# Kernel optimization log

Measured on AMD Instinct MI355X. Metric: run time of the kernel, lower is better.

The kernel has to match this reference:

```python
import jax, jax.numpy as jnp
import numpy as np

# pywt db4 reconstruction low-pass (rec_lo) coefficients.
_H = np.array([
    0.23037781330885523, 0.7148465705525415, 0.6308807679295904,
    -0.02798376941698385, -0.18703481171888114, 0.030841381835986965,
    0.032883011666982945, -0.010597401784997278], dtype=np.float64)
# pywt dec_lo = _H[::-1]; conv (flipped) correlation kernel = dec_lo[::-1] = _H.
_FLO = _H
# dec_hi[k] = (-1)^(7-k) * _H[k]; correlation kernel = dec_hi[::-1] -> (-1)^k * _H[7-k].
_FHI = np.array([(-1.0) ** k * _H[7 - k] for k in range(8)])
_FILT = jnp.asarray(np.stack([_FLO, _FHI])[:, None, :], dtype=jnp.float32)  # [2,1,8]
_PAD = 7  # filter_len - 1
_LEVEL = 4


def _dwt_step(sig):
    """One pywt dwt level, mode='symmetric'. sig: [N, L] -> (cA, cD), each [N, (L+7)//2]."""
    # symmetric (half-sample) extension by filter_len-1 each side, drop first sample
    # so that stride-2 VALID correlation reproduces pywt's output phase/length.
    xp = jnp.pad(sig, ((0, 0), (_PAD, _PAD)), mode='symmetric')[:, 1:]
    out = jax.lax.conv_general_dilated(
        xp[:, None, :], _FILT, window_strides=(2,), padding='VALID',
        dimension_numbers=('NCH', 'OIH', 'NCH'))  # [N, 2, (L+7)//2]
    return out[:, 0, :], out[:, 1, :]


def setup_inputs() -> dict:
    key = jax.random.key(0)
    x = jax.random.normal(key, (64, 4096, 32), dtype=jnp.float32)  # [B, L, C]
    return {"x": x}


def reference(x):
    """Faithful batched version of pywt.wavedec(x[i,:,j], 'db4', 'symmetric', level=4).
    Returns tuple (cA4, cD4, cD3, cD2, cD1), each [B, C, scale_len]."""
    B, L, C = x.shape
    sig = jnp.transpose(x, (0, 2, 1)).reshape(B * C, L)
    details = []
    for _ in range(_LEVEL):
        sig, cd = _dwt_step(sig)
        details.append(cd)
    coeffs = [sig] + details[::-1]  # [cA_L, cD_L, ..., cD_1] like pywt.wavedec
    return tuple(c.reshape(B, C, c.shape[-1]) for c in coeffs)
```

## Files before the change

kernel.cpp:

```cpp
#include <hip/hip_runtime.h>


#define NCH 4
#define LPX 634
#define LP1 322
#define LP2 166
#define LP3 86
#define CDPA 314
#define CDPB 154
#define CAP4 40

template <int R, bool LAST>
__device__ __forceinline__ void level_run(
    const float* __restrict__ src, int PS, int srclo,
    float* __restrict__ dst, int PD, int DL,
    int lo, int hi,
    float* __restrict__ cdbuf, int CDP,
    float* __restrict__ cabuf,
    int c, int slot) {
    constexpr float FLO[8] = {
        0.23037781330885523f,  0.7148465705525415f,  0.6308807679295904f,
        -0.02798376941698385f, -0.18703481171888114f, 0.030841381835986965f,
        0.032883011666982945f, -0.010597401784997278f};
    constexpr float FHI[8] = {
        -0.010597401784997278f, -0.032883011666982945f, 0.030841381835986965f,
        0.18703481171888114f,  -0.02798376941698385f,  -0.6308807679295904f,
        0.7148465705525415f,   -0.23037781330885523f};

    const int span = hi - lo;
    int i0r = slot * R;
    if (i0r > span - R) i0r = span - R;
    const int i0 = lo + i0r;

    const float2* row2 = reinterpret_cast<const float2*>(src + c * PS);
    int p = i0 - (srclo >> 1);
    float2 f0 = row2[p], f1 = row2[p + 1], f2 = row2[p + 2];
    float* drow = LAST ? nullptr : dst + c * PD;
    float* cdrow = cdbuf + c * CDP - lo;
    float* carow = LAST ? cabuf + c * CAP4 - lo : nullptr;

#pragma unroll
    for (int r = 0; r < R; ++r) {
        const float2 f3 = row2[p + 3 + r];
        const int i = i0 + r;
        const float w0 = f0.x, w1 = f0.y, w2 = f1.x, w3 = f1.y;
        const float w4 = f2.x, w5 = f2.y, w6 = f3.x, w7 = f3.y;
        float a = FLO[0] * w0;
        a = fmaf(FLO[1], w1, a); a = fmaf(FLO[2], w2, a); a = fmaf(FLO[3], w3, a);
        a = fmaf(FLO[4], w4, a); a = fmaf(FLO[5], w5, a); a = fmaf(FLO[6], w6, a);
        a = fmaf(FLO[7], w7, a);
        float d = FHI[0] * w0;
        d = fmaf(FHI[1], w1, d); d = fmaf(FHI[2], w2, d); d = fmaf(FHI[3], w3, d);
        d = fmaf(FHI[4], w4, d); d = fmaf(FHI[5], w5, d); d = fmaf(FHI[6], w6, d);
        d = fmaf(FHI[7], w7, d);

        if constexpr (!LAST) {
            drow[i - lo + 6] = a;
            if (lo == 0 && i < 6) drow[5 - i] = a;
            if (hi == DL && i >= DL - 7) drow[(2 * DL - 1 - i) - lo + 6] = a;
        } else {
            carow[i] = a;
        }
        cdrow[i] = d;
        f0 = f1; f1 = f2; f2 = f3;
    }
}

__device__ __forceinline__ void dump_rows(
    const float* __restrict__ buf, int pitch, int bufLo,
    float* __restrict__ gbase, int rowLen, int ownLo, int ownHi, int tid) {
    const int span = ownHi - ownLo;
#pragma unroll
    for (int c2 = 0; c2 < NCH; ++c2) {
        float* g = gbase + (size_t)c2 * rowLen + ownLo;
        const float* s = buf + c2 * pitch + (ownLo - bufLo);
        for (int i = tid; i < span; i += 256) g[i] = s[i];
    }
}

__global__ __launch_bounds__(256) void fused_dwt_kernel(
    const float* __restrict__ x, float* __restrict__ out) {
    __shared__ __align__(16) float bx[NCH * LPX];
    __shared__ __align__(16) float b1[NCH * LP1];
    __shared__ __align__(16) float b2[NCH * LP2];
    __shared__ __align__(16) float b3[NCH * LP3];
    __shared__ __align__(16) float cdA[NCH * CDPA];
    __shared__ __align__(16) float cdB[NCH * CDPB];
    __shared__ __align__(16) float caB[NCH * CAP4];

    const int bid = blockIdx.x;
    const int work = (bid & 7) * 512 + (bid >> 3);
    const int cg = work & 7;
    const int tile = (work >> 3) & 7;
    const int b = work >> 6;

    const int tid = threadIdx.x;
    const int c = tid & 3;
    const int slot = tid >> 2;
    const int c0 = cg * 4;

    const int L0 = 4096, L1 = 2051, L2 = 1029, L3 = 518, L4 = 262;

    const int lo4 = tile * 33, hi4 = min(L4, lo4 + 33);
    const int lo3 = max(0, 2 * lo4 - 6), hi3 = min(L3, 2 * hi4);
    const int lo2 = max(0, 2 * lo3 - 6), hi2 = min(L2, 2 * hi3);
    const int lo1 = max(0, 2 * lo2 - 6), hi1 = min(L1, 2 * hi2);
    const int lox = max(0, 2 * lo1 - 6), hix = min(L0, 2 * hi1);

    const float* xb = x + (size_t)b * L0 * 32 + c0;
    const int nx = hix - lox;
    for (int q = tid; q < nx; q += 256) {
        const int t = lox + q;
        const float4 v = *reinterpret_cast<const float4*>(xb + (size_t)t * 32);
        const float vv[4] = {v.x, v.y, v.z, v.w};
#pragma unroll
        for (int hh = 0; hh < 4; ++hh) {
            float* row = bx + hh * LPX;
            row[q + 6] = vv[hh];
            if (lox == 0 && t < 6) row[5 - t] = vv[hh];
            if (hix == L0 && t >= L0 - 7) row[(2 * L0 - 1 - t) - lox + 6] = vv[hh];
        }
    }
    __syncthreads();

    const size_t S = 2048;
    const size_t sigB = (size_t)b * 32 + c0;
    float* gca4 = out + sigB * L4;
    float* gcd4 = out + S * (size_t)L4 + sigB * L4;
    float* gcd3 = out + 2 * S * (size_t)L4 + sigB * L3;
    float* gcd2 = out + 2 * S * (size_t)L4 + S * (size_t)L3 + sigB * L2;
    float* gcd1 = out + 2 * S * (size_t)L4 + S * (size_t)L3 + S * (size_t)L2 + sigB * L1;

    const int o1lo = tile ? 264 * tile - 34 : 0;
    const int o1hi = (tile == 7) ? L1 : 264 * tile + 230;
    const int o2lo = tile ? 132 * tile - 10 : 0;
    const int o2hi = (tile == 7) ? L2 : 132 * tile + 122;
    const int o3lo = tile ? 66 * tile - 2 : 0;
    const int o3hi = (tile == 7) ? L3 : 66 * tile + 64;

    level_run<5, false>(bx, LPX, lox, b1, LP1, L1, lo1, hi1, cdA, CDPA, nullptr, c, slot);
    __syncthreads();

    dump_rows(cdA, CDPA, lo1, gcd1, L1, o1lo, o1hi, tid);
    level_run<3, false>(b1, LP1, lo1, b2, LP2, L2, lo2, hi2, cdB, CDPB, nullptr, c, slot);
    __syncthreads();

    dump_rows(cdB, CDPB, lo2, gcd2, L2, o2lo, o2hi, tid);
    level_run<2, false>(b2, LP2, lo2, b3, LP3, L3, lo3, hi3, cdA, CDPA, nullptr, c, slot);
    __syncthreads();

    dump_rows(cdA, CDPA, lo3, gcd3, L3, o3lo, o3hi, tid);
    level_run<1, true>(b3, LP3, lo3, nullptr, 0, L4, lo4, hi4, cdB, CDPB, caB, c, slot);
    __syncthreads();

    dump_rows(cdB, CDPB, lo4, gcd4, L4, lo4, hi4, tid);
    dump_rows(caB, CAP4, lo4, gca4, L4, lo4, hi4, tid);
}

extern "C" void kernel_launch(void* const* d_in, const int* in_sizes, int n_in,
                              void* d_out, int out_size, void* d_ws, size_t ws_size,
                              hipStream_t stream) {
    const float* x = (const float*)d_in[0];
    float* out = (float*)d_out;
    fused_dwt_kernel<<<dim3(4096), dim3(256), 0, stream>>>(x, out);
}
```

Before: 31.29 us.

## Halve channels per block to double grid size and split FIR accumulation chains

Each block now handles 2 channels instead of 4, so the grid doubles to 8192 blocks with half the shared memory per block, and launch bounds request 8 blocks per CU. The per-thread row counts per level shrink accordingly, and input loads become two float2 rows per thread instead of one float4. The 8-tap filter is split into two independent FMA chains to shorten dependency latency. The cost is narrower global reads, which use fewer bytes per 32-float row stride, and more redundant halo work per output element.

```diff
diff --git a/kernel.cpp b/kernel.cpp
--- a/kernel.cpp
+++ b/kernel.cpp
@@ -1,7 +1,9 @@
 #include <hip/hip_runtime.h>
 
 
-#define NCH 4
+#define NT 256
+#define NCHB 2
+
 #define LPX 634
 #define LP1 322
 #define LP2 166
@@ -9,6 +11,42 @@
 #define CDPA 314
 #define CDPB 154
 #define CAP4 40
+
+#define L0C 4096
+#define L1C 2051
+#define L2C 1029
+#define L3C 518
+#define L4C 262
+#define SC 2048
+
+#define OFF_CD4 (SC * L4C)
+#define OFF_CD3 (2 * SC * L4C)
+#define OFF_CD2 (OFF_CD3 + SC * L3C)
+#define OFF_CD1 (OFF_CD2 + SC * L2C)
+
+__device__ __forceinline__ void filt8(
+    const float w0, const float w1, const float w2, const float w3,
+    const float w4, const float w5, const float w6, const float w7,
+    float& a, float& d) {
+    constexpr float FLO[8] = {
+        0.23037781330885523f,  0.7148465705525415f,  0.6308807679295904f,
+        -0.02798376941698385f, -0.18703481171888114f, 0.030841381835986965f,
+        0.032883011666982945f, -0.010597401784997278f};
+    constexpr float FHI[8] = {
+        -0.010597401784997278f, -0.032883011666982945f, 0.030841381835986965f,
+        0.18703481171888114f,  -0.02798376941698385f,  -0.6308807679295904f,
+        0.7148465705525415f,   -0.23037781330885523f};
+    float a0 = FLO[0] * w0;
+    a0 = fmaf(FLO[1], w1, a0); a0 = fmaf(FLO[2], w2, a0); a0 = fmaf(FLO[3], w3, a0);
+    float a1 = FLO[4] * w4;
+    a1 = fmaf(FLO[5], w5, a1); a1 = fmaf(FLO[6], w6, a1); a1 = fmaf(FLO[7], w7, a1);
+    a = a0 + a1;
+    float d0 = FHI[0] * w0;
+    d0 = fmaf(FHI[1], w1, d0); d0 = fmaf(FHI[2], w2, d0); d0 = fmaf(FHI[3], w3, d0);
+    float d1 = FHI[4] * w4;
+    d1 = fmaf(FHI[5], w5, d1); d1 = fmaf(FHI[6], w6, d1); d1 = fmaf(FHI[7], w7, d1);
+    d = d0 + d1;
+}
 
 template <int R, bool LAST>
 __device__ __forceinline__ void level_run(
@@ -18,15 +56,6 @@
     float* __restrict__ cdbuf, int CDP,
     float* __restrict__ cabuf,
     int c, int slot) {
-    constexpr float FLO[8] = {
-        0.23037781330885523f,  0.7148465705525415f,  0.6308807679295904f,
-        -0.02798376941698385f, -0.18703481171888114f, 0.030841381835986965f,
-        0.032883011666982945f, -0.010597401784997278f};
-    constexpr float FHI[8] = {
-        -0.010597401784997278f, -0.032883011666982945f, 0.030841381835986965f,
-        0.18703481171888114f,  -0.02798376941698385f,  -0.6308807679295904f,
-        0.7148465705525415f,   -0.23037781330885523f};
-
     const int span = hi - lo;
     int i0r = slot * R;
     if (i0r > span - R) i0r = span - R;
@@ -43,16 +72,8 @@
     for (int r = 0; r < R; ++r) {
         const float2 f3 = row2[p + 3 + r];
         const int i = i0 + r;
-        const float w0 = f0.x, w1 = f0.y, w2 = f1.x, w3 = f1.y;
-        const float w4 = f2.x, w5 = f2.y, w6 = f3.x, w7 = f3.y;
-        float a = FLO[0] * w0;
-        a = fmaf(FLO[1], w1, a); a = fmaf(FLO[2], w2, a); a = fmaf(FLO[3], w3, a);
-        a = fmaf(FLO[4], w4, a); a = fmaf(FLO[5], w5, a); a = fmaf(FLO[6], w6, a);
-        a = fmaf(FLO[7], w7, a);
-        float d = FHI[0] * w0;
-        d = fmaf(FHI[1], w1, d); d = fmaf(FHI[2], w2, d); d = fmaf(FHI[3], w3, d);
-        d = fmaf(FHI[4], w4, d); d = fmaf(FHI[5], w5, d); d = fmaf(FHI[6], w6, d);
-        d = fmaf(FHI[7], w7, d);
+        float a, d;
+        filt8(f0.x, f0.y, f1.x, f1.y, f2.x, f2.y, f3.x, f3.y, a, d);
 
         if constexpr (!LAST) {
             drow[i - lo + 6] = a;
@@ -71,96 +92,107 @@
     float* __restrict__ gbase, int rowLen, int ownLo, int ownHi, int tid) {
     const int span = ownHi - ownLo;
 #pragma unroll
-    for (int c2 = 0; c2 < NCH; ++c2) {
+    for (int c2 = 0; c2 < NCHB; ++c2) {
         float* g = gbase + (size_t)c2 * rowLen + ownLo;
         const float* s = buf + c2 * pitch + (ownLo - bufLo);
-        for (int i = tid; i < span; i += 256) g[i] = s[i];
+        for (int i = tid; i < span; i += NT) g[i] = s[i];
     }
 }
 
-__global__ __launch_bounds__(256) void fused_dwt_kernel(
+__global__ __launch_bounds__(NT, 8) void fused_dwt_kernel(
     const float* __restrict__ x, float* __restrict__ out) {
-    __shared__ __align__(16) float bx[NCH * LPX];
-    __shared__ __align__(16) float b1[NCH * LP1];
-    __shared__ __align__(16) float b2[NCH * LP2];
-    __shared__ __align__(16) float b3[NCH * LP3];
-    __shared__ __align__(16) float cdA[NCH * CDPA];
-    __shared__ __align__(16) float cdB[NCH * CDPB];
-    __shared__ __align__(16) float caB[NCH * CAP4];
+    __shared__ __align__(16) float bx[NCHB * LPX];
+    __shared__ __align__(16) float b1[NCHB * LP1];
+    __shared__ __align__(16) float b2[NCHB * LP2];
+    __shared__ __align__(16) float b3[NCHB * LP3];
+    __shared__ __align__(16) float cdA[NCHB * CDPA];
+    __shared__ __align__(16) float cdB[NCHB * CDPB];
+    __shared__ __align__(16) float caB[NCHB * CAP4];
 
     const int bid = blockIdx.x;
-    const int work = (bid & 7) * 512 + (bid >> 3);
-    const int cg = work & 7;
-    const int tile = (work >> 3) & 7;
-    const int b = work >> 6;
+    const int work = (bid & 7) * 1024 + (bid >> 3);
+    const int cg = work & 15;
+    const int tile = (work >> 4) & 7;
+    const int b = work >> 7;
 
     const int tid = threadIdx.x;
-    const int c = tid & 3;
-    const int slot = tid >> 2;
-    const int c0 = cg * 4;
+    const int c = tid & 1;
+    const int slot = tid >> 1;
+    const int c0 = cg * 2;
+    const int sigB = b * 32 + c0;
 
-    const int L0 = 4096, L1 = 2051, L2 = 1029, L3 = 518, L4 = 262;
+    const int lo4 = 33 * tile, hi4 = min(L4C, lo4 + 33);
+    const int lo3 = max(0, 2 * lo4 - 6), hi3 = min(L3C, 2 * hi4);
+    const int lo2 = max(0, 2 * lo3 - 6), hi2 = min(L2C, 2 * hi3);
+    const int lo1 = max(0, 2 * lo2 - 6), hi1 = min(L1C, 2 * hi2);
+    const int lox = max(0, 2 * lo1 - 6), hix = min(L0C, 2 * hi1);
 
-    const int lo4 = tile * 33, hi4 = min(L4, lo4 + 33);
-    const int lo3 = max(0, 2 * lo4 - 6), hi3 = min(L3, 2 * hi4);
-    const int lo2 = max(0, 2 * lo3 - 6), hi2 = min(L2, 2 * hi3);
-    const int lo1 = max(0, 2 * lo2 - 6), hi1 = min(L1, 2 * hi2);
-    const int lox = max(0, 2 * lo1 - 6), hix = min(L0, 2 * hi1);
-
-    const float* xb = x + (size_t)b * L0 * 32 + c0;
-    const int nx = hix - lox;
-    for (int q = tid; q < nx; q += 256) {
-        const int t = lox + q;
-        const float4 v = *reinterpret_cast<const float4*>(xb + (size_t)t * 32);
-        const float vv[4] = {v.x, v.y, v.z, v.w};
+    const float* xb = x + (size_t)b * (L0C * 32) + c0;
+    const int npair = (hix - lox) >> 1;
+    for (int q = tid; q < npair; q += NT) {
+        const int j = q << 1;
+        const int t = lox + j;
+        const float2 va = *reinterpret_cast<const float2*>(xb + (size_t)t * 32);
+        const float2 vb = *reinterpret_cast<const float2*>(xb + (size_t)(t + 1) * 32);
+        const float avv[2] = {va.x, va.y};
+        const float bvv[2] = {vb.x, vb.y};
 #pragma unroll
-        for (int hh = 0; hh < 4; ++hh) {
-            float* row = bx + hh * LPX;
-            row[q + 6] = vv[hh];
-            if (lox == 0 && t < 6) row[5 - t] = vv[hh];
-            if (hix == L0 && t >= L0 - 7) row[(2 * L0 - 1 - t) - lox + 6] = vv[hh];
+        for (int hh = 0; hh < NCHB; ++hh)
+            *reinterpret_cast<float2*>(bx + hh * LPX + 6 + j) = make_float2(avv[hh], bvv[hh]);
+        if (lox == 0 && t < 6) {
+#pragma unroll
+            for (int hh = 0; hh < NCHB; ++hh) {
+                bx[hh * LPX + 5 - t] = avv[hh];
+                if (t + 1 < 6) bx[hh * LPX + 4 - t] = bvv[hh];
+            }
+        }
+        if (hix == L0C && t + 1 >= L0C - 7) {
+#pragma unroll
+            for (int hh = 0; hh < NCHB; ++hh) {
+                if (t >= L0C - 7) bx[hh * LPX + (2 * L0C - 1 - t) - lox + 6] = avv[hh];
+                bx[hh * LPX + (2 * L0C - 2 - t) - lox + 6] = bvv[hh];
+            }
         }
     }
     __syncthreads();
 
-    const size_t S = 2048;
-    const size_t sigB = (size_t)b * 32 + c0;
-    float* gca4 = out + sigB * L4;
-    float* gcd4 = out + S * (size_t)L4 + sigB * L4;
-    float* gcd3 = out + 2 * S * (size_t)L4 + sigB * L3;
-    float* gcd2 = out + 2 * S * (size_t)L4 + S * (size_t)L3 + sigB * L2;
-    float* gcd1 = out + 2 * S * (size_t)L4 + S * (size_t)L3 + S * (size_t)L2 + sigB * L1;
+    float* gca4 = out + (size_t)sigB * L4C;
+    float* gcd4 = out + OFF_CD4 + (size_t)sigB * L4C;
+    float* gcd3 = out + OFF_CD3 + (size_t)sigB * L3C;
+    float* gcd2 = out + OFF_CD2 + (size_t)sigB * L2C;
+    float* gcd1 = out + OFF_CD1 + (size_t)sigB * L1C;
 
     const int o1lo = tile ? 264 * tile - 34 : 0;
-    const int o1hi = (tile == 7) ? L1 : 264 * tile + 230;
+    const int o1hi = (tile == 7) ? L1C : 264 * tile + 230;
     const int o2lo = tile ? 132 * tile - 10 : 0;
-    const int o2hi = (tile == 7) ? L2 : 132 * tile + 122;
+    const int o2hi = (tile == 7) ? L2C : 132 * tile + 122;
     const int o3lo = tile ? 66 * tile - 2 : 0;
-    const int o3hi = (tile == 7) ? L3 : 66 * tile + 64;
+    const int o3hi = (tile == 7) ? L3C : 66 * tile + 64;
 
-    level_run<5, false>(bx, LPX, lox, b1, LP1, L1, lo1, hi1, cdA, CDPA, nullptr, c, slot);
+    level_run<3, false>(bx, LPX, lox, b1, LP1, L1C, lo1, hi1, cdA, CDPA, nullptr, c, slot);
     __syncthreads();
 
-    dump_rows(cdA, CDPA, lo1, gcd1, L1, o1lo, o1hi, tid);
-    level_run<3, false>(b1, LP1, lo1, b2, LP2, L2, lo2, hi2, cdB, CDPB, nullptr, c, slot);
+    dump_rows(cdA, CDPA, lo1, gcd1, L1C, o1lo, o1hi, tid);
+    level_run<2, false>(b1, LP1, lo1, b2, LP2, L2C, lo2, hi2, cdB, CDPB, nullptr, c, slot);
     __syncthreads();
 
-    dump_rows(cdB, CDPB, lo2, gcd2, L2, o2lo, o2hi, tid);
-    level_run<2, false>(b2, LP2, lo2, b3, LP3, L3, lo3, hi3, cdA, CDPA, nullptr, c, slot);
+    dump_rows(cdB, CDPB, lo2, gcd2, L2C, o2lo, o2hi, tid);
+    level_run<1, false>(b2, LP2, lo2, b3, LP3, L3C, lo3, hi3, cdA, CDPA, nullptr, c, slot);
     __syncthreads();
 
-    dump_rows(cdA, CDPA, lo3, gcd3, L3, o3lo, o3hi, tid);
-    level_run<1, true>(b3, LP3, lo3, nullptr, 0, L4, lo4, hi4, cdB, CDPB, caB, c, slot);
+    dump_rows(cdA, CDPA, lo3, gcd3, L3C, o3lo, o3hi, tid);
+    level_run<1, true>(b3, LP3, lo3, nullptr, 0, L4C, lo4, hi4, cdB, CDPB, caB, c, slot);
     __syncthreads();
 
-    dump_rows(cdB, CDPB, lo4, gcd4, L4, lo4, hi4, tid);
-    dump_rows(caB, CAP4, lo4, gca4, L4, lo4, hi4, tid);
+    dump_rows(cdB, CDPB, lo4, gcd4, L4C, lo4, hi4, tid);
+    dump_rows(caB, CAP4, lo4, gca4, L4C, lo4, hi4, tid);
 }
 
 extern "C" void kernel_launch(void* const* d_in, const int* in_sizes, int n_in,
                               void* d_out, int out_size, void* d_ws, size_t ws_size,
                               hipStream_t stream) {
+    (void)in_sizes; (void)n_in; (void)d_ws; (void)ws_size; (void)out_size;
     const float* x = (const float*)d_in[0];
     float* out = (float*)d_out;
-    fused_dwt_kernel<<<dim3(4096), dim3(256), 0, stream>>>(x, out);
+    fused_dwt_kernel<<<dim3(8192), dim3(NT), 0, stream>>>(x, out);
 }
```

Result: slower. 32.88 us (+5.1%).
